# Kernel optimization log

Measured on AMD Instinct MI355X. Metric: run time of the kernel, lower is better.

## Reference

```python
import jax, jax.numpy as jnp
import numpy as np

B, S, D = 2, 2048, 2048
H, KVH = 32, 8
HD = D // H            # 64
G = H // KVH           # 4 query heads per kv head
CLIP = 8.0
THETA = 500000.0
EPS = 1e-6
SCALE = 1.0 / np.sqrt(HD)


def setup_inputs() -> dict:
    key = jax.random.key(0)
    ks = jax.random.split(key, 4)
    hidden_states = jax.random.normal(ks[0], (B, S, D), dtype=jnp.float32)
    attention_mask = jnp.ones((B, S), dtype=jnp.int32)
    position_ids = jnp.broadcast_to(jnp.arange(S, dtype=jnp.int32)[None, :], (B, S))
    causal_mask = jnp.tril(jnp.ones((S, S), dtype=bool))[None, None]
    std = 0.02
    w_qkv = jax.random.normal(ks[1], (D, D + 2 * KVH * HD), dtype=jnp.float32) * std
    w_out = jax.random.normal(ks[2], (D, D), dtype=jnp.float32) * std
    ln1_scale = jnp.ones((D,), dtype=jnp.float32)
    ln2_scale = jnp.ones((D,), dtype=jnp.float32)
    return {
        "hidden_states": hidden_states,
        "attention_mask": attention_mask,
        "position_ids": position_ids,
        "causal_mask": causal_mask,
        "ln1_scale": ln1_scale,
        "w_qkv": w_qkv,
        "w_out": w_out,
        "ln2_scale": ln2_scale,
    }


def _layernorm(x, scale):
    m = jnp.mean(x, axis=-1, keepdims=True)
    v = jnp.mean(jnp.square(x - m), axis=-1, keepdims=True)
    return (x - m) * jax.lax.rsqrt(v + EPS) * scale


def _rope(x, cos, sin):
    # neox style: rotate halves of head_dim. x: [B,S,h,HD], cos/sin: [B,S,1,HD/2]
    x1, x2 = jnp.split(x, 2, axis=-1)
    return jnp.concatenate([x1 * cos - x2 * sin, x2 * cos + x1 * sin], axis=-1)


def _forward(hidden_states, attention_mask, position_ids, causal_mask,
             ln1_scale, w_qkv, w_out, ln2_scale):
    residual = hidden_states
    x = _layernorm(hidden_states, ln1_scale)

    qkv = jnp.clip(x @ w_qkv, -CLIP, CLIP)  # [B,S,D+2*KVH*HD]
    q, kv = jnp.split(qkv, [D], axis=2)
    k, v = jnp.split(kv, [KVH * HD], axis=2)
    q = q.reshape(B, S, H, HD)
    k = k.reshape(B, S, KVH, HD)
    v = v.reshape(B, S, KVH, HD)

    inv_freq = 1.0 / (THETA ** (jnp.arange(0, HD, 2, dtype=jnp.float32) / HD))
    ang = position_ids.astype(jnp.float32)[..., None] * inv_freq  # [B,S,HD/2]
    cos = jnp.cos(ang)[:, :, None, :]
    sin = jnp.sin(ang)[:, :, None, :]
    q = _rope(q, cos, sin)
    k = _rope(k, cos, sin)

    # GQA: group query heads per kv head
    qg = q.reshape(B, S, KVH, G, HD)
    scores = jnp.einsum("bqhgd,bkhd->bhgqk", qg, k) * SCALE  # [B,KVH,G,S,S]
    mask = causal_mask[:, :, :S, :S] & (attention_mask[:, None, None, :] > 0)  # [B,1,S,S]
    bias = jnp.where(mask[:, :, None], 0.0, jnp.finfo(scores.dtype).min)
    probs = jax.nn.softmax(scores + bias, axis=-1)
    attn = jnp.einsum("bhgqk,bkhd->bqhgd", probs, v).reshape(B, S, D)

    attn_out = attn @ w_out
    hidden = attn_out + residual
    residual2 = hidden
    hidden = _layernorm(hidden, ln2_scale)
    return residual2, hidden


def reference(hidden_states, attention_mask, position_ids, causal_mask,
              ln1_scale, w_qkv, w_out, ln2_scale):
    return _forward(hidden_states, attention_mask, position_ids, causal_mask,
                    ln1_scale, w_qkv, w_out, ln2_scale)
```

## Files before the change

### kernel.cpp

```cpp
#include <hip/hip_runtime.h>
#include <hip/hip_bf16.h>
#include <stdint.h>

typedef __bf16 bf16_t;
typedef __bf16 bf16x8 __attribute__((ext_vector_type(8)));
typedef float f32x4 __attribute__((ext_vector_type(4)));
typedef _Float16 f16x8v __attribute__((ext_vector_type(8)));
typedef _Float16 f16x4v __attribute__((ext_vector_type(4)));

#define LOG2E 1.44269504088896f

__device__ __forceinline__ void load_lds16(const void* g, void* l) {
  __builtin_amdgcn_global_load_lds(
      (__attribute__((address_space(1))) unsigned int*)(uintptr_t)(g),
      (__attribute__((address_space(3))) unsigned int*)(l),
      16, 0, 0);
}

__device__ __forceinline__ f16x4v pack4_f16(float a, float b, float c, float d) {
  const __fp16 __attribute__((ext_vector_type(2))) lo = __builtin_amdgcn_cvt_pkrtz(a, b);
  const __fp16 __attribute__((ext_vector_type(2))) hi = __builtin_amdgcn_cvt_pkrtz(c, d);
  return __builtin_bit_cast(f16x4v, __builtin_shufflevector(lo, hi, 0, 1, 2, 3));
}

__global__ __launch_bounds__(256) void ln_kernel(
    const float* __restrict__ in, const float* __restrict__ gamma,
    bf16_t* __restrict__ out_bf, float* __restrict__ out_f)
{
  const int row = blockIdx.x;
  const int t = threadIdx.x;
  const float* x = in + (size_t)row * 2048;
  float4 a = ((const float4*)x)[t];
  float4 b = ((const float4*)x)[t + 256];
  float v[8] = {a.x, a.y, a.z, a.w, b.x, b.y, b.z, b.w};
  float s = 0.f, q = 0.f;
#pragma unroll
  for (int i = 0; i < 8; ++i) { s += v[i]; q += v[i] * v[i]; }
#pragma unroll
  for (int off = 1; off < 64; off <<= 1) {
    s += __shfl_xor(s, off, 64);
    q += __shfl_xor(q, off, 64);
  }
  __shared__ float red[4][2];
  if ((t & 63) == 0) { red[t >> 6][0] = s; red[t >> 6][1] = q; }
  __syncthreads();
  s = red[0][0] + red[1][0] + red[2][0] + red[3][0];
  q = red[0][1] + red[1][1] + red[2][1] + red[3][1];
  const float mean = s * (1.0f / 2048.0f);
  const float var = q * (1.0f / 2048.0f) - mean * mean;
  const float inv = rsqrtf(var + 1e-6f);
  float4 ga = ((const float4*)gamma)[t];
  float4 gb = ((const float4*)gamma)[t + 256];
  float g[8] = {ga.x, ga.y, ga.z, ga.w, gb.x, gb.y, gb.z, gb.w};
  float y[8];
#pragma unroll
  for (int i = 0; i < 8; ++i) y[i] = (v[i] - mean) * inv * g[i];
  if (out_bf) {
    alignas(16) bf16_t tb[8];
#pragma unroll
    for (int i = 0; i < 8; ++i) tb[i] = (bf16_t)y[i];
    bf16_t* o = out_bf + (size_t)row * 2048;
    *(uint2*)(o + t * 4) = *(const uint2*)(tb);
    *(uint2*)(o + (t + 256) * 4) = *(const uint2*)(tb + 4);
  } else {
    float* o = out_f + (size_t)row * 2048;
    ((float4*)o)[t] = make_float4(y[0], y[1], y[2], y[3]);
    ((float4*)o)[t + 256] = make_float4(y[4], y[5], y[6], y[7]);
  }
}

__global__ __launch_bounds__(256) void fused_pre(
    const float* __restrict__ hid, const float* __restrict__ ln1g,
    bf16_t* __restrict__ xb,
    const float* __restrict__ wqkv, const float* __restrict__ wout,
    bf16_t* __restrict__ wT, bf16_t* __restrict__ wOT,
    float2* __restrict__ tbl)
{
  const int bid = blockIdx.x;
  const int t = threadIdx.x;
  if (bid < 4096) {
    const float* x = hid + (size_t)bid * 2048;
    float4 a = ((const float4*)x)[t];
    float4 b = ((const float4*)x)[t + 256];
    float v[8] = {a.x, a.y, a.z, a.w, b.x, b.y, b.z, b.w};
    float s = 0.f, q = 0.f;
#pragma unroll
    for (int i = 0; i < 8; ++i) { s += v[i]; q += v[i] * v[i]; }
#pragma unroll
    for (int off = 1; off < 64; off <<= 1) {
      s += __shfl_xor(s, off, 64);
      q += __shfl_xor(q, off, 64);
    }
    __shared__ float red[4][2];
    if ((t & 63) == 0) { red[t >> 6][0] = s; red[t >> 6][1] = q; }
    __syncthreads();
    s = red[0][0] + red[1][0] + red[2][0] + red[3][0];
    q = red[0][1] + red[1][1] + red[2][1] + red[3][1];
    const float mean = s * (1.0f / 2048.0f);
    const float var = q * (1.0f / 2048.0f) - mean * mean;
    const float inv = rsqrtf(var + 1e-6f);
    float4 ga = ((const float4*)ln1g)[t];
    float4 gb = ((const float4*)ln1g)[t + 256];
    float g[8] = {ga.x, ga.y, ga.z, ga.w, gb.x, gb.y, gb.z, gb.w};
    alignas(16) bf16_t tb[8];
#pragma unroll
    for (int i = 0; i < 8; ++i) tb[i] = (bf16_t)((v[i] - mean) * inv * g[i]);
    bf16_t* o = xb + (size_t)bid * 2048;
    *(uint2*)(o + t * 4) = *(const uint2*)(tb);
    *(uint2*)(o + (t + 256) * 4) = *(const uint2*)(tb + 4);
    return;
  }
  if (bid >= 14336) {
    const int idx = (bid - 14336) * 256 + t;
    const int p = idx >> 5, i = idx & 31;
    const float inv = exp2f(-0.59161151f * (float)i);
    float sn, cs;
    sincosf((float)p * inv, &sn, &cs);
    tbl[idx] = make_float2(cs, sn);
    return;
  }
  const bool isQ = bid < 10240;
  const int i6 = isQ ? (bid - 4096) : (bid - 10240);
  const int bx = isQ ? (i6 % 96) : (i6 & 63);
  const int by = isQ ? (i6 / 96) : (i6 >> 6);
  const float* in = isQ ? wqkv : wout;
  bf16_t* out = isQ ? wT : wOT;
  const int in_stride = isQ ? 3072 : 2048;
  const int c0 = bx * 32, r0 = by * 32;
  const int tx = t & 31, ty = t >> 5;
  __shared__ float tile[32][33];
#pragma unroll
  for (int i = 0; i < 4; ++i)
    tile[ty + i * 8][tx] = in[(size_t)(r0 + ty + i * 8) * in_stride + c0 + tx];
  __syncthreads();
#pragma unroll
  for (int i = 0; i < 4; ++i)
    out[(size_t)(c0 + ty + i * 8) * 2048 + r0 + tx] = (bf16_t)tile[tx][ty + i * 8];
}

__global__ __launch_bounds__(256) void rope_v(
    const _Float16* __restrict__ qkv, const int* __restrict__ pos_ids,
    const float2* __restrict__ tbl,
    _Float16* __restrict__ qo, _Float16* __restrict__ ko,
    _Float16* __restrict__ vt)
{
  const int bid = blockIdx.x;
  const int t = threadIdx.x;
  __shared__ float tile[32][33];
  if (bid < 4096) {
    const int b = bid >> 11, s = bid & 2047;
    const float2* tp = tbl + (size_t)pos_ids[bid] * 32;
    const _Float16* row = qkv + (size_t)bid * 3072;
    const float qsc = 0.125f * LOG2E;
#pragma unroll
    for (int pp = 0; pp < 4; ++pp) {
      const int p = t + pp * 256;
      const int hh = p >> 5, i = p & 31;
      const float2 cssn = tp[i];
      const float x1 = (float)row[hh * 64 + i];
      const float x2 = (float)row[hh * 64 + 32 + i];
      _Float16* d = qo + (((size_t)b * 32 + hh) * 2048 + s) * 64 + i;
      d[0] = (_Float16)((x1 * cssn.x - x2 * cssn.y) * qsc);
      d[32] = (_Float16)((x2 * cssn.x + x1 * cssn.y) * qsc);
    }
    {
      const int hh = t >> 5, i = t & 31;
      const float2 cssn = tp[i];
      const float x1 = (float)row[2048 + hh * 64 + i];
      const float x2 = (float)row[2048 + hh * 64 + 32 + i];
      _Float16* d = ko + (((size_t)b * 8 + hh) * 2048 + s) * 64 + i;
      d[0] = (_Float16)(x1 * cssn.x - x2 * cssn.y);
      d[32] = (_Float16)(x2 * cssn.x + x1 * cssn.y);
    }
    return;
  }
  const int idx = bid - 4096;
  const int bz = idx >> 10;
  const int rem = idx & 1023;
  const int bx = rem & 15, by = rem >> 4;
  const _Float16* ib = qkv + 2560 + (size_t)bz * 2048 * 3072;
  _Float16* ob = vt + (size_t)bz * 512 * 2048;
  const int c0 = bx * 32, r0 = by * 32;
  const int tx = t & 31, ty = t >> 5;
#pragma unroll
  for (int i = 0; i < 4; ++i)
    tile[ty + i * 8][tx] = (float)ib[(size_t)(r0 + ty + i * 8) * 3072 + c0 + tx];
  __syncthreads();
#pragma unroll
  for (int i = 0; i < 4; ++i)
    ob[(size_t)(c0 + ty + i * 8) * 2048 + r0 + tx] = (_Float16)tile[tx][ty + i * 8];
}

__global__ __launch_bounds__(256) void gemm_bt(
    const bf16_t* __restrict__ A, const bf16_t* __restrict__ BT,
    int M, int N, int K, int mode,
    const float* __restrict__ resid, void* __restrict__ outv)
{
  __shared__ alignas(16) bf16_t As[128 * 32];
  __shared__ alignas(16) bf16_t Bs[128 * 32];
  const int t = threadIdx.x;
  const int lane = t & 63;
  const int wave = t >> 6;
  const int m0 = blockIdx.y * 128;
  const int n0 = blockIdx.x * 128;
  const int wm = (wave >> 1) * 64;
  const int wn = (wave & 1) * 64;

  f32x4 acc[4][4] = {};

  const int i0 = t, i1 = t + 256;
  const bf16_t* Ag0 = A + (size_t)(m0 + (i0 >> 2)) * K + (i0 & 3) * 8;
  const bf16_t* Ag1 = A + (size_t)(m0 + (i1 >> 2)) * K + (i1 & 3) * 8;
  const bf16_t* Bg0 = BT + (size_t)(n0 + (i0 >> 2)) * K + (i0 & 3) * 8;
  const bf16_t* Bg1 = BT + (size_t)(n0 + (i1 >> 2)) * K + (i1 & 3) * 8;
  bf16_t* AsW0 = As + (size_t)(wave * 64) * 8;
  bf16_t* AsW1 = As + (size_t)(256 + wave * 64) * 8;
  bf16_t* BsW0 = Bs + (size_t)(wave * 64) * 8;
  bf16_t* BsW1 = Bs + (size_t)(256 + wave * 64) * 8;

  const int rsel = lane & 15;
  const int ksel = (lane >> 4) * 8;

  for (int k0 = 0; k0 < K; k0 += 32) {
    __syncthreads();
    load_lds16(Ag0 + k0, AsW0);
    load_lds16(Ag1 + k0, AsW1);
    load_lds16(Bg0 + k0, BsW0);
    load_lds16(Bg1 + k0, BsW1);
    __syncthreads();
    bf16x8 af[4], bfr[4];
#pragma unroll
    for (int i = 0; i < 4; ++i) {
      af[i]  = *(const bf16x8*)(As + (wm + i * 16 + rsel) * 32 + ksel);
      bfr[i] = *(const bf16x8*)(Bs + (wn + i * 16 + rsel) * 32 + ksel);
    }
#pragma unroll
    for (int mi = 0; mi < 4; ++mi)
#pragma unroll
      for (int ni = 0; ni < 4; ++ni)
        acc[mi][ni] = __builtin_amdgcn_mfma_f32_16x16x32_bf16(af[mi], bfr[ni], acc[mi][ni], 0, 0, 0);
  }

  const int row_l = (lane >> 4) * 4;
  const int col_l = lane & 15;
#pragma unroll
  for (int mi = 0; mi < 4; ++mi) {
#pragma unroll
    for (int ni = 0; ni < 4; ++ni) {
      const size_t base = (size_t)(m0 + wm + mi * 16 + row_l) * N + (size_t)(n0 + wn + ni * 16 + col_l);
#pragma unroll
      for (int r = 0; r < 4; ++r) {
        float vv = acc[mi][ni][r];
        if (mode == 0) {
          vv = fminf(8.0f, fmaxf(-8.0f, vv));
          ((_Float16*)outv)[base + (size_t)r * N] = (_Float16)vv;
        } else {
          ((float*)outv)[base + (size_t)r * N] = vv + resid[base + (size_t)r * N];
        }
      }
    }
  }
}

#define STAGE_TO(J, SI) do { \
    _Float16* d_ = &KV[(SI)][ksel][wv4]; \
    const _Float16* s_ = gsrc + (size_t)(J) * gstep; \
    load_lds16(s_, d_); \
    load_lds16(s_ + 32, d_ + 2048); \
  } while (0)

#define ABODY(J, BI, SI) do { \
    const int j_ = (J); \
    if (j_ == nit - 1) asm volatile("s_waitcnt vmcnt(0)" ::: "memory"); \
    else               asm volatile("s_waitcnt vmcnt(2)" ::: "memory"); \
    __builtin_amdgcn_s_barrier(); \
    __builtin_amdgcn_sched_barrier(0); \
    if (j_ + 2 < nit) STAGE_TO(j_ + 2, SI); \
    const _Float16* Kbuf = &KV[(BI)][0][0]; \
    const _Float16* Vbuf = &KV[(BI)][1][0]; \
    f32x4 st[4] = {}; \
    __builtin_amdgcn_s_setprio(1); \
    _Pragma("unroll") \
    for (int mt_ = 0; mt_ < 4; ++mt_) { \
      const f16x8v kf0_ = *(const f16x8v*)(Kbuf + krowc[mt_]); \
      const f16x8v kf1_ = *(const f16x8v*)(Kbuf + 2048 + krowc[mt_]); \
      st[mt_] = __builtin_amdgcn_mfma_f32_16x16x32_f16(kf0_, qf0, st[mt_], 0, 0, 0); \
      st[mt_] = __builtin_amdgcn_mfma_f32_16x16x32_f16(kf1_, qf1, st[mt_], 0, 0, 0); \
    } \
    __builtin_amdgcn_s_setprio(0); \
     \
    f16x4v vA_[4], vB_[4], vC_[4], vD_[4]; \
    _Pragma("unroll") \
    for (int nt_ = 0; nt_ < 4; ++nt_) { \
      const _Float16* Vr_ = Vbuf + vrow[nt_]; \
      vA_[nt_] = *(const f16x4v*)(Vr_ + vca); \
      vB_[nt_] = *(const f16x4v*)(Vr_ + vcb); \
      vC_[nt_] = *(const f16x4v*)(Vr_ + 2048 + vca); \
      vD_[nt_] = *(const f16x4v*)(Vr_ + 2048 + vcb); \
    } \
    const int k0_ = j_ * 64; \
    if (k0_ + 64 > q0) { \
      _Pragma("unroll") \
      for (int mt_ = 0; mt_ < 4; ++mt_) \
        _Pragma("unroll") \
        for (int r_ = 0; r_ < 4; ++r_) { \
          if (k0_ + mt_ * 16 + lg * 4 + r_ > myq) st[mt_][r_] = -3.0e38f; \
        } \
    } \
     \
    const float x0_ = fmaxf(fmaxf(st[0][0], st[0][1]), st[0][2]); \
    const float x1_ = fmaxf(fmaxf(st[0][3], st[1][0]), st[1][1]); \
    const float x2_ = fmaxf(fmaxf(st[1][2], st[1][3]), st[2][0]); \
    const float x3_ = fmaxf(fmaxf(st[2][1], st[2][2]), st[2][3]); \
    const float x4_ = fmaxf(fmaxf(st[3][0], st[3][1]), st[3][2]); \
    float mx_ = fmaxf(fmaxf(fmaxf(x0_, x1_), fmaxf(x2_, x3_)), fmaxf(x4_, st[3][3])); \
    if (__any(mx_ > m_r + 8.0f)) {   \
      mx_ = fmaxf(mx_, __shfl_xor(mx_, 16, 64)); \
      mx_ = fmaxf(mx_, __shfl_xor(mx_, 32, 64)); \
      const float mn_ = fmaxf(m_r, mx_); \
      const float al_ = exp2f(m_r - mn_); \
      _Pragma("unroll") \
      for (int r_ = 0; r_ < 4; ++r_) { \
        const float ao_ = __shfl(al_, lg * 4 + r_, 16); \
        ov[0][r_] *= ao_; ov[1][r_] *= ao_; ov[2][r_] *= ao_; ov[3][r_] *= ao_; \
        ovl[r_] *= ao_; \
      } \
      m_r = mn_; \
    } \
    f16x4v pf_[4]; \
    _Pragma("unroll") \
    for (int mt_ = 0; mt_ < 4; ++mt_) { \
      pf_[mt_] = pack4_f16(exp2f(st[mt_][0] - m_r), exp2f(st[mt_][1] - m_r), \
                           exp2f(st[mt_][2] - m_r), exp2f(st[mt_][3] - m_r)); \
    } \
    __builtin_amdgcn_s_setprio(1); \
    _Pragma("unroll") \
    for (int nt_ = 0; nt_ < 4; ++nt_) { \
      ov[nt_] = __builtin_amdgcn_mfma_f32_16x16x16f16(pf_[0], vA_[nt_], ov[nt_], 0, 0, 0); \
      ov[nt_] = __builtin_amdgcn_mfma_f32_16x16x16f16(pf_[1], vB_[nt_], ov[nt_], 0, 0, 0); \
      ov[nt_] = __builtin_amdgcn_mfma_f32_16x16x16f16(pf_[2], vC_[nt_], ov[nt_], 0, 0, 0); \
      ov[nt_] = __builtin_amdgcn_mfma_f32_16x16x16f16(pf_[3], vD_[nt_], ov[nt_], 0, 0, 0); \
    } \
    ovl = __builtin_amdgcn_mfma_f32_16x16x16f16(pf_[0], onesv, ovl, 0, 0, 0); \
    ovl = __builtin_amdgcn_mfma_f32_16x16x16f16(pf_[1], onesv, ovl, 0, 0, 0); \
    ovl = __builtin_amdgcn_mfma_f32_16x16x16f16(pf_[2], onesv, ovl, 0, 0, 0); \
    ovl = __builtin_amdgcn_mfma_f32_16x16x16f16(pf_[3], onesv, ovl, 0, 0, 0); \
    __builtin_amdgcn_s_setprio(0); \
  } while (0)

__global__ __launch_bounds__(512, 4) void attn_kernel(
    const _Float16* __restrict__ Q, const _Float16* __restrict__ Kb,
    const _Float16* __restrict__ Vt, bf16_t* __restrict__ Out)
{
  __shared__ alignas(16) _Float16 KV[3][2][4096];

  const int kvh = blockIdx.y;
  const int b = blockIdx.z;
  const int t = threadIdx.x;
  const int lane = t & 63;
  const int wave = t >> 6;
  const int g = wave >> 1;
  const int tile = wave & 1;
  const int h = kvh * 4 + g;
  const int ln15 = lane & 15;
  const int lg = lane >> 4;

  const _Float16* Qh = Q + ((size_t)(b * 32 + h) * 2048) * 64;
  const _Float16* Kh = Kb + ((size_t)(b * 8 + kvh) * 2048) * 64;
  const _Float16* Vh = Vt + ((size_t)(b * 8 + kvh) * 64) * 2048;

  const bool stK = (t < 256);
  const int u = t & 255;
  const int srow = u >> 2;
  const int scol = ((u & 3) ^ ((srow >> 1) & 3)) * 8;
  const _Float16* gsrc = stK ? (Kh + (size_t)srow * 64 + scol)
                             : (Vh + (size_t)srow * 2048 + scol);
  const int gstep = stK ? 64 * 64 : 64;
  const int ksel = stK ? 0 : 1;
  const int wv4 = (wave & 3) * 512;

  const int svz = (ln15 >> 1) & 3;
  const int kc = (lg ^ svz) * 8;
  const int vca = ((lg >> 1) ^ svz) * 8 + (lg & 1) * 4;
  const int vcb = (((lg >> 1) + 2) ^ svz) * 8 + (lg & 1) * 4;
  int krowc[4], vrow[4];
#pragma unroll
  for (int i = 0; i < 4; ++i) {
    krowc[i] = (i * 16 + ln15) * 32 + kc;
    vrow[i] = (i * 16 + ln15) * 32;
  }
  const f16x4v onesv = {(_Float16)1.0f, (_Float16)1.0f, (_Float16)1.0f, (_Float16)1.0f};

  for (int half = 0; half < 2; ++half) {
    const int qc = (half == 0) ? blockIdx.x : (63 - blockIdx.x);
    const int q0 = qc * 32 + tile * 16;
    const int myq = q0 + ln15;
    const int nit = (qc >> 1) + 1;

    const f16x8v qf0 = *(const f16x8v*)(Qh + (size_t)(q0 + ln15) * 64 + lg * 8);
    const f16x8v qf1 = *(const f16x8v*)(Qh + (size_t)(q0 + ln15) * 64 + 32 + lg * 8);

    f32x4 ov[4] = {};
    f32x4 ovl = {};
    float m_r = 0.0f;

    STAGE_TO(0, 0);
    if (nit > 1) STAGE_TO(1, 1);

    int it = 0;
    for (; it + 3 <= nit; it += 3) {
      ABODY(it, 0, 2);
      ABODY(it + 1, 1, 0);
      ABODY(it + 2, 2, 1);
    }
    if (it < nit) { ABODY(it, 0, 2); ++it; }
    if (it < nit) { ABODY(it, 1, 0); }

#pragma unroll
    for (int r = 0; r < 4; ++r) {
      const float ilo = 1.0f / ovl[r];
      const size_t obase = ((size_t)b * 2048 + (size_t)(q0 + lg * 4 + r)) * 2048 + (size_t)h * 64;
#pragma unroll
      for (int nt = 0; nt < 4; ++nt)
        Out[obase + nt * 16 + ln15] = (bf16_t)(ov[nt][r] * ilo);
    }
    __builtin_amdgcn_s_barrier();
    __builtin_amdgcn_sched_barrier(0);
  }
}
#undef ABODY
#undef STAGE_TO

extern "C" void kernel_launch(void* const* d_in, const int* in_sizes, int n_in,
                              void* d_out, int out_size, void* d_ws, size_t ws_size,
                              hipStream_t stream) {
  (void)in_sizes; (void)n_in; (void)out_size; (void)ws_size;
  const float* hid  = (const float*)d_in[0];
  const int*   pos  = (const int*)d_in[2];
  const float* ln1g = (const float*)d_in[4];
  const float* wqkv = (const float*)d_in[5];
  const float* wout = (const float*)d_in[6];
  const float* ln2g = (const float*)d_in[7];
  float* out = (float*)d_out;
  char* ws = (char*)d_ws;

  bf16_t*   xb  = (bf16_t*)(ws + 0);
  bf16_t*   wT  = (bf16_t*)(ws + 16777216);
  _Float16* qkv = (_Float16*)(ws + 29360128);
  float2*   tbl = (float2*)(ws + 54525952);
  bf16_t*   wOT = (bf16_t*)(ws + 55050240);
  _Float16* qb  = (_Float16*)(ws + 79691776);
  _Float16* kb  = (_Float16*)(ws + 96468992);
  _Float16* vt  = (_Float16*)(ws + 100663296);

  fused_pre<<<14592, 256, 0, stream>>>(hid, ln1g, xb, wqkv, wout, wT, wOT, tbl);
  gemm_bt<<<dim3(24, 32), 256, 0, stream>>>(xb, wT, 4096, 3072, 2048, 0, nullptr, qkv);
  rope_v<<<6144, 256, 0, stream>>>(qkv, pos, tbl, qb, kb, vt);
  attn_kernel<<<dim3(32, 8, 2), 512, 0, stream>>>(qb, kb, vt, xb);
  gemm_bt<<<dim3(16, 32), 256, 0, stream>>>(xb, wOT, 4096, 2048, 2048, 1, hid, out);
  ln_kernel<<<4096, 256, 0, stream>>>(out, ln2g, nullptr, out + 8388608);
}
```

Baseline: 374.6 us.

## Fuse Q rotary embedding into attention and vectorize K/V prep and transposes

Drops the separate Q rope pass and its intermediate Q buffer. The attention kernel now reads raw Q straight from the qkv buffer and applies rope and the softmax scale in registers when it loads each query tile. K rope and the V transpose stay in a smaller prep kernel, now using 8-wide half loads and stores. The weight and V transposes switch to float4 or 4-wide loads and 8-byte stores. This saves a full write and re-read of Q in exchange for a little extra work and table lookups at the start of attention.

```diff
diff --git a/kernel.cpp b/kernel.cpp
--- a/kernel.cpp
+++ b/kernel.cpp
@@ -127,68 +127,66 @@
   bf16_t* out = isQ ? wT : wOT;
   const int in_stride = isQ ? 3072 : 2048;
   const int c0 = bx * 32, r0 = by * 32;
-  const int tx = t & 31, ty = t >> 5;
   __shared__ float tile[32][33];
-#pragma unroll
-  for (int i = 0; i < 4; ++i)
-    tile[ty + i * 8][tx] = in[(size_t)(r0 + ty + i * 8) * in_stride + c0 + tx];
+  const int r = t >> 3, c4 = (t & 7) * 4;
+  const float4 v4 = *(const float4*)(in + (size_t)(r0 + r) * in_stride + c0 + c4);
+  tile[r][c4] = v4.x; tile[r][c4 + 1] = v4.y;
+  tile[r][c4 + 2] = v4.z; tile[r][c4 + 3] = v4.w;
   __syncthreads();
-#pragma unroll
-  for (int i = 0; i < 4; ++i)
-    out[(size_t)(c0 + ty + i * 8) * 2048 + r0 + tx] = (bf16_t)tile[tx][ty + i * 8];
-}
-
-__global__ __launch_bounds__(256) void rope_v(
+  const int cc = t >> 3, rr4 = (t & 7) * 4;
+  alignas(8) bf16_t obuf[4];
+#pragma unroll
+  for (int j = 0; j < 4; ++j) obuf[j] = (bf16_t)tile[rr4 + j][cc];
+  *(uint2*)(out + (size_t)(c0 + cc) * 2048 + r0 + rr4) = *(const uint2*)obuf;
+}
+
+__global__ __launch_bounds__(256) void kv_prep(
     const _Float16* __restrict__ qkv, const int* __restrict__ pos_ids,
     const float2* __restrict__ tbl,
-    _Float16* __restrict__ qo, _Float16* __restrict__ ko,
-    _Float16* __restrict__ vt)
+    _Float16* __restrict__ ko, _Float16* __restrict__ vt)
 {
   const int bid = blockIdx.x;
   const int t = threadIdx.x;
-  __shared__ float tile[32][33];
-  if (bid < 4096) {
-    const int b = bid >> 11, s = bid & 2047;
-    const float2* tp = tbl + (size_t)pos_ids[bid] * 32;
-    const _Float16* row = qkv + (size_t)bid * 3072;
-    const float qsc = 0.125f * LOG2E;
-#pragma unroll
-    for (int pp = 0; pp < 4; ++pp) {
-      const int p = t + pp * 256;
-      const int hh = p >> 5, i = p & 31;
-      const float2 cssn = tp[i];
-      const float x1 = (float)row[hh * 64 + i];
-      const float x2 = (float)row[hh * 64 + 32 + i];
-      _Float16* d = qo + (((size_t)b * 32 + hh) * 2048 + s) * 64 + i;
-      d[0] = (_Float16)((x1 * cssn.x - x2 * cssn.y) * qsc);
-      d[32] = (_Float16)((x2 * cssn.x + x1 * cssn.y) * qsc);
-    }
-    {
-      const int hh = t >> 5, i = t & 31;
-      const float2 cssn = tp[i];
-      const float x1 = (float)row[2048 + hh * 64 + i];
-      const float x2 = (float)row[2048 + hh * 64 + 32 + i];
-      _Float16* d = ko + (((size_t)b * 8 + hh) * 2048 + s) * 64 + i;
-      d[0] = (_Float16)(x1 * cssn.x - x2 * cssn.y);
-      d[32] = (_Float16)(x2 * cssn.x + x1 * cssn.y);
-    }
+  if (bid < 512) {
+    const int lr = t >> 5, u = t & 31;
+    const int bs = bid * 8 + lr;
+    const int b = bs >> 11, s = bs & 2047;
+    const int hh = u >> 2, i8 = (u & 3) * 8;
+    const _Float16* row = qkv + (size_t)bs * 3072 + 2048 + hh * 64;
+    const float2* tp = tbl + (size_t)pos_ids[bs] * 32 + i8;
+    const f16x8v x1v = *(const f16x8v*)(row + i8);
+    const f16x8v x2v = *(const f16x8v*)(row + 32 + i8);
+    f16x8v y1, y2;
+#pragma unroll
+    for (int j = 0; j < 8; ++j) {
+      const float2 cs = tp[j];
+      const float x1 = (float)x1v[j], x2 = (float)x2v[j];
+      y1[j] = (_Float16)(x1 * cs.x - x2 * cs.y);
+      y2[j] = (_Float16)(x2 * cs.x + x1 * cs.y);
+    }
+    _Float16* d = ko + (((size_t)b * 8 + hh) * 2048 + s) * 64 + i8;
+    *(f16x8v*)(d) = y1;
+    *(f16x8v*)(d + 32) = y2;
     return;
   }
-  const int idx = bid - 4096;
+  const int idx = bid - 512;
   const int bz = idx >> 10;
   const int rem = idx & 1023;
   const int bx = rem & 15, by = rem >> 4;
-  const _Float16* ib = qkv + 2560 + (size_t)bz * 2048 * 3072;
+  const _Float16* ib = qkv + (size_t)bz * 2048 * 3072 + 2560;
   _Float16* ob = vt + (size_t)bz * 512 * 2048;
   const int c0 = bx * 32, r0 = by * 32;
-  const int tx = t & 31, ty = t >> 5;
-#pragma unroll
-  for (int i = 0; i < 4; ++i)
-    tile[ty + i * 8][tx] = (float)ib[(size_t)(r0 + ty + i * 8) * 3072 + c0 + tx];
+  __shared__ float tile[32][33];
+  const int r = t >> 3, c4 = (t & 7) * 4;
+  const f16x4v v4 = *(const f16x4v*)(ib + (size_t)(r0 + r) * 3072 + c0 + c4);
+#pragma unroll
+  for (int j = 0; j < 4; ++j) tile[r][c4 + j] = (float)v4[j];
   __syncthreads();
-#pragma unroll
-  for (int i = 0; i < 4; ++i)
-    ob[(size_t)(c0 + ty + i * 8) * 2048 + r0 + tx] = (_Float16)tile[tx][ty + i * 8];
+  const int cc = t >> 3, rr4 = (t & 7) * 4;
+  alignas(8) _Float16 obuf[4];
+#pragma unroll
+  for (int j = 0; j < 4; ++j) obuf[j] = (_Float16)tile[rr4 + j][cc];
+  *(uint2*)(ob + (size_t)(c0 + cc) * 2048 + r0 + rr4) = *(const uint2*)obuf;
 }
 
 __global__ __launch_bounds__(256) void gemm_bt(
@@ -349,8 +347,10 @@
   } while (0)
 
 __global__ __launch_bounds__(512, 4) void attn_kernel(
-    const _Float16* __restrict__ Q, const _Float16* __restrict__ Kb,
-    const _Float16* __restrict__ Vt, bf16_t* __restrict__ Out)
+    const _Float16* __restrict__ qkv, const int* __restrict__ pos,
+    const float2* __restrict__ tbl,
+    const _Float16* __restrict__ Kb, const _Float16* __restrict__ Vt,
+    bf16_t* __restrict__ Out)
 {
   __shared__ alignas(16) _Float16 KV[3][2][4096];
 
@@ -365,7 +365,6 @@
   const int ln15 = lane & 15;
   const int lg = lane >> 4;
 
-  const _Float16* Qh = Q + ((size_t)(b * 32 + h) * 2048) * 64;
   const _Float16* Kh = Kb + ((size_t)(b * 8 + kvh) * 2048) * 64;
   const _Float16* Vh = Vt + ((size_t)(b * 8 + kvh) * 64) * 2048;
 
@@ -390,6 +389,7 @@
     vrow[i] = (i * 16 + ln15) * 32;
   }
   const f16x4v onesv = {(_Float16)1.0f, (_Float16)1.0f, (_Float16)1.0f, (_Float16)1.0f};
+  const float qsc = 0.125f * LOG2E;
 
   for (int half = 0; half < 2; ++half) {
     const int qc = (half == 0) ? blockIdx.x : (63 - blockIdx.x);
@@ -397,8 +397,18 @@
     const int myq = q0 + ln15;
     const int nit = (qc >> 1) + 1;
 
-    const f16x8v qf0 = *(const f16x8v*)(Qh + (size_t)(q0 + ln15) * 64 + lg * 8);
-    const f16x8v qf1 = *(const f16x8v*)(Qh + (size_t)(q0 + ln15) * 64 + 32 + lg * 8);
+    const _Float16* qrow = qkv + (size_t)(b * 2048 + myq) * 3072 + h * 64;
+    const float2* tq = tbl + (size_t)pos[b * 2048 + myq] * 32 + lg * 8;
+    const f16x8v qr0 = *(const f16x8v*)(qrow + lg * 8);
+    const f16x8v qr1 = *(const f16x8v*)(qrow + 32 + lg * 8);
+    f16x8v qf0, qf1;
+#pragma unroll
+    for (int j = 0; j < 8; ++j) {
+      const float2 cs = tq[j];
+      const float x1 = (float)qr0[j], x2 = (float)qr1[j];
+      qf0[j] = (_Float16)((x1 * cs.x - x2 * cs.y) * qsc);
+      qf1[j] = (_Float16)((x2 * cs.x + x1 * cs.y) * qsc);
+    }
 
     f32x4 ov[4] = {};
     f32x4 ovl = {};
@@ -449,14 +459,13 @@
   _Float16* qkv = (_Float16*)(ws + 29360128);
   float2*   tbl = (float2*)(ws + 54525952);
   bf16_t*   wOT = (bf16_t*)(ws + 55050240);
-  _Float16* qb  = (_Float16*)(ws + 79691776);
-  _Float16* kb  = (_Float16*)(ws + 96468992);
-  _Float16* vt  = (_Float16*)(ws + 100663296);
+  _Float16* kb  = (_Float16*)(ws + 79691776);
+  _Float16* vt  = (_Float16*)(ws + 83886080);
 
   fused_pre<<<14592, 256, 0, stream>>>(hid, ln1g, xb, wqkv, wout, wT, wOT, tbl);
   gemm_bt<<<dim3(24, 32), 256, 0, stream>>>(xb, wT, 4096, 3072, 2048, 0, nullptr, qkv);
-  rope_v<<<6144, 256, 0, stream>>>(qkv, pos, tbl, qb, kb, vt);
-  attn_kernel<<<dim3(32, 8, 2), 512, 0, stream>>>(qb, kb, vt, xb);
+  kv_prep<<<2560, 256, 0, stream>>>(qkv, pos, tbl, kb, vt);
+  attn_kernel<<<dim3(32, 8, 2), 512, 0, stream>>>(qkv, pos, tbl, kb, vt, xb);
   gemm_bt<<<dim3(16, 32), 256, 0, stream>>>(xb, wOT, 4096, 2048, 2048, 1, hid, out);
   ln_kernel<<<4096, 256, 0, stream>>>(out, ln2g, nullptr, out + 8388608);
 }
```

Result: faster. 358.6 us (-4.3%).
